# Optimization experiments

Measured on AMD Instinct MI355X. Metric: run time of the kernel, lower is better.

## Reference

```python
import jax, jax.numpy as jnp
import numpy as np

B, S, D, N, C = 32, 1024, 256, 32, 64
ROUTING_ITERS = 3


def setup_inputs() -> dict:
    key = jax.random.key(0)
    k1, k2 = jax.random.split(key)
    x = jax.random.normal(k1, (B, S, D), dtype=jnp.float32)
    W = jax.random.normal(k2, (N, D, C), dtype=jnp.float32) * 0.1
    return {"x": x, "W": W}


def _squash(s, eps=1e-8):
    # s: [B, N, C]; squash along last dim
    sq_norm = jnp.sum(s * s, axis=-1, keepdims=True)
    return (sq_norm / (1.0 + sq_norm)) * s / jnp.sqrt(sq_norm + eps)


def reference(x, W):
    # Prediction vectors: u_hat[b,s,n,c] = sum_d x[b,s,d] * W[n,d,c]
    u_hat = jnp.einsum('bsd,ndc->bsnc', x, W)  # [B, S, N, C]
    b_logits = jnp.zeros(u_hat.shape[:3], dtype=u_hat.dtype)  # [B, S, N]
    v = None
    for i in range(ROUTING_ITERS):
        c = jax.nn.softmax(b_logits, axis=2)               # [B, S, N]
        s = jnp.einsum('bsn,bsnc->bnc', c, u_hat)          # [B, N, C]
        v = _squash(s)                                      # [B, N, C]
        if i < ROUTING_ITERS - 1:
            agreement = jnp.einsum('bsnc,bnc->bsn', u_hat, v)
            b_logits = b_logits + agreement
    return v
```

## Files before the change

### kernel.cpp

```cpp
#include <hip/hip_runtime.h>
#include <math.h>

namespace {
constexpr int B_ = 32, S_ = 1024, D_ = 256, N_ = 32, C_ = 64;
constexpr int NC_ = N_ * C_;
constexpr int XP_ = 16;

typedef __bf16 bf16x8 __attribute__((ext_vector_type(8)));
typedef __bf16 bf16x4 __attribute__((ext_vector_type(4)));
typedef float floatx4 __attribute__((ext_vector_type(4)));

constexpr int XS_ = 264;
constexpr int TS_ = 264;
constexpr int CS_ = 72;
}

extern "C" __global__ __launch_bounds__(256) void k_stage(
    const float* __restrict__ x, float* __restrict__ xsum_part,
    __bf16* __restrict__ xb_ws) {
  const int b = blockIdx.x, sb = blockIdx.y, t = threadIdx.x;
  const float* xb = x + ((size_t)b * S_ + sb * 64) * D_;
  float a = 0.f;
  #pragma unroll 8
  for (int s = 0; s < 64; ++s) a += xb[s * D_ + t];
  xsum_part[((size_t)b * XP_ + sb) * D_ + t] = a;

  __bf16* xo = xb_ws + ((size_t)(b * XP_ + sb)) * (64 * D_);
  #pragma unroll
  for (int i = 0; i < 16; ++i) {
    int pos = i * 1024 + t * 4;
    float4 f = *(const float4*)(xb + pos);
    bf16x4 p4;
    p4[0] = (__bf16)f.x; p4[1] = (__bf16)f.y;
    p4[2] = (__bf16)f.z; p4[3] = (__bf16)f.w;
    *(bf16x4*)(xo + pos) = p4;
  }
}

extern "C" __global__ __launch_bounds__(256) void k_small(
    const float* __restrict__ z, const float* __restrict__ W,
    float* __restrict__ t_fp, __bf16* __restrict__ t_bhi,
    __bf16* __restrict__ t_blo, float* __restrict__ vout,
    float* __restrict__ yzero,
    int P, int zb, int zp, int zn, float scale, int accum, int final_) {
  __shared__ float zloc[256];
  __shared__ float sq_red[4][64];
  __shared__ float v_lds[64];
  const int b = blockIdx.x, n = blockIdx.y, t = threadIdx.x;

  float a = 0.f;
  for (int p = 0; p < P; ++p) a += z[(size_t)b * zb + (size_t)p * zp + n * zn + t];
  zloc[t] = a;
  if (yzero) yzero[((size_t)b * N_ + n) * D_ + t] = 0.f;
  __syncthreads();

  const int c = t & 63, dq = t >> 6;
  const float* Wn = W + (size_t)n * (D_ * C_);
  float s = 0.f;
  #pragma unroll 8
  for (int dd = 0; dd < 64; ++dd) {
    int d = dq * 64 + dd;
    s += zloc[d] * Wn[d * 64 + c];
  }
  sq_red[dq][c] = s;
  __syncthreads();

  if (t < 64) {
    float sc = (sq_red[0][t] + sq_red[1][t] + sq_red[2][t] + sq_red[3][t]) * scale;
    float sq = sc * sc;
    #pragma unroll
    for (int m = 1; m <= 32; m <<= 1) sq += __shfl_xor(sq, m);
    float scl = sq / ((1.f + sq) * sqrtf(sq + 1e-8f));
    float v = sc * scl;
    v_lds[t] = v;
    if (final_) vout[(size_t)b * NC_ + n * 64 + t] = v;
  }
  __syncthreads();

  if (!final_) {
    const float4* W4 = (const float4*)Wn + t * 16;
    float acc = 0.f;
    #pragma unroll
    for (int q = 0; q < 16; ++q) {
      float4 wv = W4[q];
      acc += wv.x * v_lds[q * 4] + wv.y * v_lds[q * 4 + 1] +
             wv.z * v_lds[q * 4 + 2] + wv.w * v_lds[q * 4 + 3];
    }
    size_t idx = ((size_t)b * N_ + n) * D_ + t;
    float tf = acc + (accum ? t_fp[idx] : 0.f);
    t_fp[idx] = tf;
    __bf16 hi = (__bf16)tf;
    t_bhi[idx] = hi;
    t_blo[idx] = (__bf16)(tf - (float)hi);
  }
}

extern "C" __global__ __launch_bounds__(256) void k_pass(
    const __bf16* __restrict__ xb_ws, const __bf16* __restrict__ t_bhi,
    const __bf16* __restrict__ t_blo, float* __restrict__ y) {
  __shared__ __align__(16) __bf16 x_lds[64 * XS_];
  __shared__ __align__(16) __bf16 th_lds[N_ * TS_];
  __shared__ __align__(16) __bf16 tl_lds[N_ * TS_];
  __shared__ __align__(16) __bf16 c_Th[N_ * CS_];
  __shared__ __align__(16) __bf16 c_Tl[N_ * CS_];
  const int b = blockIdx.x, ch = blockIdx.y;
  const int t = threadIdx.x, w = t >> 6, lane = t & 63;
  const int quad = lane >> 4, l16 = lane & 15;

  #pragma unroll
  for (int e = 0; e < 4; ++e) {
    int idx = e * 2048 + t * 8;
    int n = idx >> 8, d = idx & 255;
    *(uint4*)(th_lds + n * TS_ + d) = *(const uint4*)(t_bhi + (size_t)b * 8192 + idx);
    *(uint4*)(tl_lds + n * TS_ + d) = *(const uint4*)(t_blo + (size_t)b * 8192 + idx);
  }
  const __bf16* xsrc = xb_ws + ((size_t)(b * XP_ + ch)) * (64 * D_);
  #pragma unroll
  for (int e = 0; e < 8; ++e) {
    int idx = e * 2048 + t * 8;
    int row = idx >> 8, col = idx & 255;
    *(uint4*)(x_lds + row * XS_ + col) = *(const uint4*)(xsrc + idx);
  }
  __syncthreads();

  floatx4 acc[2];
  acc[0] = (floatx4){0.f, 0.f, 0.f, 0.f};
  acc[1] = (floatx4){0.f, 0.f, 0.f, 0.f};
  const int sbase = w * 16;
  #pragma unroll
  for (int k0 = 0; k0 < 256; k0 += 32) {
    int ks = k0 + quad * 8;
    bf16x8 bfrag = *(const bf16x8*)(x_lds + (sbase + l16) * XS_ + ks);
    #pragma unroll
    for (int i = 0; i < 2; ++i) {
      bf16x8 ah = *(const bf16x8*)(th_lds + (i * 16 + l16) * TS_ + ks);
      bf16x8 al = *(const bf16x8*)(tl_lds + (i * 16 + l16) * TS_ + ks);
      acc[i] = __builtin_amdgcn_mfma_f32_16x16x32_bf16(ah, bfrag, acc[i], 0, 0, 0);
      acc[i] = __builtin_amdgcn_mfma_f32_16x16x32_bf16(al, bfrag, acc[i], 0, 0, 0);
    }
  }
  float mx = -1e30f;
  #pragma unroll
  for (int i = 0; i < 2; ++i)
    #pragma unroll
    for (int r = 0; r < 4; ++r) mx = fmaxf(mx, acc[i][r]);
  mx = fmaxf(mx, __shfl_xor(mx, 16));
  mx = fmaxf(mx, __shfl_xor(mx, 32));
  float e_[2][4];
  float ss = 0.f;
  #pragma unroll
  for (int i = 0; i < 2; ++i)
    #pragma unroll
    for (int r = 0; r < 4; ++r) { e_[i][r] = __expf(acc[i][r] - mx); ss += e_[i][r]; }
  ss += __shfl_xor(ss, 16);
  ss += __shfl_xor(ss, 32);
  float inv = 1.f / ss;
  #pragma unroll
  for (int i = 0; i < 2; ++i)
    #pragma unroll
    for (int r = 0; r < 4; ++r) {
      float cv = e_[i][r] * inv;
      __bf16 chi = (__bf16)cv;
      int o = (i * 16 + quad * 4 + r) * CS_ + sbase + l16;
      c_Th[o] = chi;
      c_Tl[o] = (__bf16)(cv - (float)chi);
    }
  __syncthreads();

  floatx4 acc2[2][4];
  #pragma unroll
  for (int i = 0; i < 2; ++i)
    #pragma unroll
    for (int dt = 0; dt < 4; ++dt) acc2[i][dt] = (floatx4){0.f, 0.f, 0.f, 0.f};
  const int dbase = w * 64;
  #pragma unroll
  for (int k0 = 0; k0 < 64; k0 += 32) {
    int ks = k0 + quad * 8;
    bf16x8 ah[2], al[2];
    #pragma unroll
    for (int i = 0; i < 2; ++i) {
      ah[i] = *(const bf16x8*)(c_Th + (i * 16 + l16) * CS_ + ks);
      al[i] = *(const bf16x8*)(c_Tl + (i * 16 + l16) * CS_ + ks);
    }
    #pragma unroll
    for (int dt = 0; dt < 4; ++dt) {
      bf16x8 bfr;
      #pragma unroll
      for (int j8 = 0; j8 < 8; ++j8)
        bfr[j8] = x_lds[(ks + j8) * XS_ + dbase + dt * 16 + l16];
      #pragma unroll
      for (int i = 0; i < 2; ++i) {
        acc2[i][dt] = __builtin_amdgcn_mfma_f32_16x16x32_bf16(ah[i], bfr, acc2[i][dt], 0, 0, 0);
        acc2[i][dt] = __builtin_amdgcn_mfma_f32_16x16x32_bf16(al[i], bfr, acc2[i][dt], 0, 0, 0);
      }
    }
  }
  #pragma unroll
  for (int i = 0; i < 2; ++i)
    #pragma unroll
    for (int dt = 0; dt < 4; ++dt)
      #pragma unroll
      for (int r = 0; r < 4; ++r) {
        int n = i * 16 + quad * 4 + r;
        int d = dbase + dt * 16 + l16;
        atomicAdd(&y[((size_t)b * N_ + n) * D_ + d], acc2[i][dt][r]);
      }
}

extern "C" void kernel_launch(void* const* d_in, const int* in_sizes, int n_in,
                              void* d_out, int out_size, void* d_ws, size_t ws_size,
                              hipStream_t stream) {
  const float* x = (const float*)d_in[0];
  const float* W = (const float*)d_in[1];
  float* out = (float*)d_out;

  char* ws = (char*)d_ws;
  __bf16* xb_ws = (__bf16*)ws;
  float* xsum_part = (float*)(ws + 16777216);
  float* y1 = (float*)(ws + 16777216 + 524288);
  float* y2 = y1 + B_ * N_ * D_;
  float* t_fp = y2 + B_ * N_ * D_;
  __bf16* t_bhi = (__bf16*)(t_fp + B_ * N_ * D_);
  __bf16* t_blo = t_bhi + B_ * N_ * D_;

  k_stage<<<dim3(B_, XP_), 256, 0, stream>>>(x, xsum_part, xb_ws);

  k_small<<<dim3(B_, N_), 256, 0, stream>>>(
      xsum_part, W, t_fp, t_bhi, t_blo, nullptr, y1,
      XP_, XP_ * D_, D_, 0, 1.f / 32.f, 0, 0);

  k_pass<<<dim3(B_, XP_), 256, 0, stream>>>(xb_ws, t_bhi, t_blo, y1);

  k_small<<<dim3(B_, N_), 256, 0, stream>>>(
      y1, W, t_fp, t_bhi, t_blo, nullptr, y2,
      1, N_ * D_, 0, D_, 1.f, 1, 0);

  k_pass<<<dim3(B_, XP_), 256, 0, stream>>>(xb_ws, t_bhi, t_blo, y2);

  k_small<<<dim3(B_, N_), 256, 0, stream>>>(
      y2, W, t_fp, t_bhi, t_blo, out, nullptr,
      1, N_ * D_, 0, D_, 1.f, 0, 1);
}
```

Baseline: 157.9 us.

## Drop bf16 staging copy of x and read routing tiles directly from global

Removes the bf16 conversion pass over x in the staging kernel; each routing pass now loads fp32 x and converts to bf16 in-kernel. The per-batch routing-logit hi/lo tiles are no longer copied into LDS and are read directly from global memory inside the MFMA loop. This eliminates a 16 MB workspace write and cuts LDS footprint, but doubles x bytes read per pass and puts global-latency loads in the inner matrix loop.

```diff
diff --git a/kernel.cpp b/kernel.cpp
--- a/kernel.cpp
+++ b/kernel.cpp
@@ -11,30 +11,17 @@
 typedef float floatx4 __attribute__((ext_vector_type(4)));
 
 constexpr int XS_ = 264;
-constexpr int TS_ = 264;
 constexpr int CS_ = 72;
 }
 
 extern "C" __global__ __launch_bounds__(256) void k_stage(
-    const float* __restrict__ x, float* __restrict__ xsum_part,
-    __bf16* __restrict__ xb_ws) {
+    const float* __restrict__ x, float* __restrict__ xsum_part) {
   const int b = blockIdx.x, sb = blockIdx.y, t = threadIdx.x;
   const float* xb = x + ((size_t)b * S_ + sb * 64) * D_;
   float a = 0.f;
   #pragma unroll 8
   for (int s = 0; s < 64; ++s) a += xb[s * D_ + t];
   xsum_part[((size_t)b * XP_ + sb) * D_ + t] = a;
-
-  __bf16* xo = xb_ws + ((size_t)(b * XP_ + sb)) * (64 * D_);
-  #pragma unroll
-  for (int i = 0; i < 16; ++i) {
-    int pos = i * 1024 + t * 4;
-    float4 f = *(const float4*)(xb + pos);
-    bf16x4 p4;
-    p4[0] = (__bf16)f.x; p4[1] = (__bf16)f.y;
-    p4[2] = (__bf16)f.z; p4[3] = (__bf16)f.w;
-    *(bf16x4*)(xo + pos) = p4;
-  }
 }
 
 extern "C" __global__ __launch_bounds__(256) void k_small(
@@ -96,33 +83,30 @@
 }
 
 extern "C" __global__ __launch_bounds__(256) void k_pass(
-    const __bf16* __restrict__ xb_ws, const __bf16* __restrict__ t_bhi,
+    const float* __restrict__ x, const __bf16* __restrict__ t_bhi,
     const __bf16* __restrict__ t_blo, float* __restrict__ y) {
   __shared__ __align__(16) __bf16 x_lds[64 * XS_];
-  __shared__ __align__(16) __bf16 th_lds[N_ * TS_];
-  __shared__ __align__(16) __bf16 tl_lds[N_ * TS_];
   __shared__ __align__(16) __bf16 c_Th[N_ * CS_];
   __shared__ __align__(16) __bf16 c_Tl[N_ * CS_];
   const int b = blockIdx.x, ch = blockIdx.y;
   const int t = threadIdx.x, w = t >> 6, lane = t & 63;
   const int quad = lane >> 4, l16 = lane & 15;
 
-  #pragma unroll
-  for (int e = 0; e < 4; ++e) {
-    int idx = e * 2048 + t * 8;
-    int n = idx >> 8, d = idx & 255;
-    *(uint4*)(th_lds + n * TS_ + d) = *(const uint4*)(t_bhi + (size_t)b * 8192 + idx);
-    *(uint4*)(tl_lds + n * TS_ + d) = *(const uint4*)(t_blo + (size_t)b * 8192 + idx);
-  }
-  const __bf16* xsrc = xb_ws + ((size_t)(b * XP_ + ch)) * (64 * D_);
-  #pragma unroll
-  for (int e = 0; e < 8; ++e) {
-    int idx = e * 2048 + t * 8;
-    int row = idx >> 8, col = idx & 255;
-    *(uint4*)(x_lds + row * XS_ + col) = *(const uint4*)(xsrc + idx);
-  }
-  __syncthreads();
-
+  const float* xb = x + ((size_t)b * S_ + ch * 64) * D_;
+  #pragma unroll
+  for (int i = 0; i < 16; ++i) {
+    int pos = i * 1024 + t * 4;
+    int row = pos >> 8, col = pos & 255;
+    float4 f = *(const float4*)(xb + row * D_ + col);
+    bf16x4 p4;
+    p4[0] = (__bf16)f.x; p4[1] = (__bf16)f.y;
+    p4[2] = (__bf16)f.z; p4[3] = (__bf16)f.w;
+    *(bf16x4*)(x_lds + row * XS_ + col) = p4;
+  }
+  __syncthreads();
+
+  const __bf16* tb_h = t_bhi + (size_t)b * 8192;
+  const __bf16* tb_l = t_blo + (size_t)b * 8192;
   floatx4 acc[2];
   acc[0] = (floatx4){0.f, 0.f, 0.f, 0.f};
   acc[1] = (floatx4){0.f, 0.f, 0.f, 0.f};
@@ -133,8 +117,8 @@
     bf16x8 bfrag = *(const bf16x8*)(x_lds + (sbase + l16) * XS_ + ks);
     #pragma unroll
     for (int i = 0; i < 2; ++i) {
-      bf16x8 ah = *(const bf16x8*)(th_lds + (i * 16 + l16) * TS_ + ks);
-      bf16x8 al = *(const bf16x8*)(tl_lds + (i * 16 + l16) * TS_ + ks);
+      bf16x8 ah = *(const bf16x8*)(tb_h + (i * 16 + l16) * 256 + ks);
+      bf16x8 al = *(const bf16x8*)(tb_l + (i * 16 + l16) * 256 + ks);
       acc[i] = __builtin_amdgcn_mfma_f32_16x16x32_bf16(ah, bfrag, acc[i], 0, 0, 0);
       acc[i] = __builtin_amdgcn_mfma_f32_16x16x32_bf16(al, bfrag, acc[i], 0, 0, 0);
     }
@@ -215,27 +199,26 @@
   float* out = (float*)d_out;
 
   char* ws = (char*)d_ws;
-  __bf16* xb_ws = (__bf16*)ws;
-  float* xsum_part = (float*)(ws + 16777216);
-  float* y1 = (float*)(ws + 16777216 + 524288);
+  float* xsum_part = (float*)ws;
+  float* y1 = (float*)(ws + 524288);
   float* y2 = y1 + B_ * N_ * D_;
   float* t_fp = y2 + B_ * N_ * D_;
   __bf16* t_bhi = (__bf16*)(t_fp + B_ * N_ * D_);
   __bf16* t_blo = t_bhi + B_ * N_ * D_;
 
-  k_stage<<<dim3(B_, XP_), 256, 0, stream>>>(x, xsum_part, xb_ws);
+  k_stage<<<dim3(B_, XP_), 256, 0, stream>>>(x, xsum_part);
 
   k_small<<<dim3(B_, N_), 256, 0, stream>>>(
       xsum_part, W, t_fp, t_bhi, t_blo, nullptr, y1,
       XP_, XP_ * D_, D_, 0, 1.f / 32.f, 0, 0);
 
-  k_pass<<<dim3(B_, XP_), 256, 0, stream>>>(xb_ws, t_bhi, t_blo, y1);
+  k_pass<<<dim3(B_, XP_), 256, 0, stream>>>(x, t_bhi, t_blo, y1);
 
   k_small<<<dim3(B_, N_), 256, 0, stream>>>(
       y1, W, t_fp, t_bhi, t_blo, nullptr, y2,
       1, N_ * D_, 0, D_, 1.f, 1, 0);
 
-  k_pass<<<dim3(B_, XP_), 256, 0, stream>>>(xb_ws, t_bhi, t_blo, y2);
+  k_pass<<<dim3(B_, XP_), 256, 0, stream>>>(x, t_bhi, t_blo, y2);
 
   k_small<<<dim3(B_, N_), 256, 0, stream>>>(
       y2, W, t_fp, t_bhi, t_blo, out, nullptr,
```

Result: slower. 173.0 us (+9.5%).
